# Kernel tuning notes

Hardware: AMD Instinct MI355X
Metric: run time of the kernel (lower is better)

Reference implementation:

```python
import jax, jax.numpy as jnp
import numpy as np
from jax import lax

B, T, C = 8, 2048, 1024
H, N = 16, 64          # n_head, head_size (C = H*N)
FFN = 3584             # dim_ffn = int(1024*3.5//32*32)
HSD = 8.0              # head_size_divisor
EPS = 1e-5


def setup_inputs() -> dict:
    key = jax.random.key(0)
    ks = jax.random.split(key, 24)
    s = 0.02
    return {
        'x': jax.random.normal(ks[0], (B, T, C), jnp.float32),
        'ln0_w': jnp.ones((C,), jnp.float32), 'ln0_b': jnp.zeros((C,), jnp.float32),
        'ln1_w': jnp.ones((C,), jnp.float32), 'ln1_b': jnp.zeros((C,), jnp.float32),
        'ln2_w': jnp.ones((C,), jnp.float32), 'ln2_b': jnp.zeros((C,), jnp.float32),
        'att_tmk': jax.random.uniform(ks[1], (C,), jnp.float32),
        'att_tmv': jax.random.uniform(ks[2], (C,), jnp.float32),
        'att_tmr': jax.random.uniform(ks[3], (C,), jnp.float32),
        'att_tmg': jax.random.uniform(ks[4], (C,), jnp.float32),
        'att_decay': jax.random.uniform(ks[5], (H, N), jnp.float32, -6.0, -1.0),
        'att_faaaa': jax.random.normal(ks[6], (H, N), jnp.float32) * 0.1,
        'att_Wr': jax.random.normal(ks[7], (C, C), jnp.float32) * s,
        'att_Wk': jax.random.normal(ks[8], (C, C), jnp.float32) * s,
        'att_Wv': jax.random.normal(ks[9], (C, C), jnp.float32) * s,
        'att_Wg': jax.random.normal(ks[10], (C, C), jnp.float32) * s,
        'att_Wo': jax.random.normal(ks[11], (C, C), jnp.float32) * s,
        'att_lnx_w': jnp.ones((C,), jnp.float32), 'att_lnx_b': jnp.zeros((C,), jnp.float32),
        'ffn_tmk': jax.random.uniform(ks[12], (C,), jnp.float32),
        'ffn_tmr': jax.random.uniform(ks[13], (C,), jnp.float32),
        'ffn_Wk': jax.random.normal(ks[14], (FFN, C), jnp.float32) * s,
        'ffn_Wr': jax.random.normal(ks[15], (C, C), jnp.float32) * s,
        'ffn_Wv': jax.random.normal(ks[16], (C, FFN), jnp.float32) * s,
    }


def token_shift(x):
    # nn.ZeroPad2d((0,0,1,-1)): shift right by one along T with zero front pad
    return jnp.pad(x, ((0, 0), (1, 0), (0, 0)))[:, :-1, :]


def layer_norm(x, w, b):
    mu = jnp.mean(x, -1, keepdims=True)
    var = jnp.var(x, -1, keepdims=True)
    return (x - mu) * lax.rsqrt(var + EPS) * w + b


def group_norm(x, w, b):
    # GroupNorm(H groups) over channel dim C = H*N
    xg = x.reshape(*x.shape[:-1], H, N)
    mu = jnp.mean(xg, -1, keepdims=True)
    var = jnp.var(xg, -1, keepdims=True)
    xg = (xg - mu) * lax.rsqrt(var + EPS)
    return xg.reshape(x.shape) * w + b


def wkv5(r, k, v, w, u):
    # r,k,v: [B,T,C]; w,u: [H,N]. Per-head decayed linear attention recurrence.
    ew = jnp.exp(-jnp.exp(w))  # [H,N] decay in (0,1)
    rt = r.reshape(B, T, H, N).transpose(1, 0, 2, 3)  # [T,B,H,N]
    kt = k.reshape(B, T, H, N).transpose(1, 0, 2, 3)
    vt = v.reshape(B, T, H, N).transpose(1, 0, 2, 3)

    def step(S, rkv):
        r_, k_, v_ = rkv                                   # [B,H,N]
        a = k_[..., :, None] * v_[..., None, :]            # [B,H,N,N] outer k v^T
        y = jnp.einsum('bhi,bhij->bhj', r_, S + u[:, :, None] * a)
        S = ew[None, :, :, None] * S + a
        return S, y

    S0 = jnp.zeros((B, H, N, N), r.dtype)
    _, ys = lax.scan(step, S0, (rt, kt, vt))               # ys: [T,B,H,N]
    return ys.transpose(1, 0, 2, 3).reshape(B, T, C)


def reference(x, ln0_w, ln0_b, ln1_w, ln1_b, ln2_w, ln2_b,
              att_tmk, att_tmv, att_tmr, att_tmg, att_decay, att_faaaa,
              att_Wr, att_Wk, att_Wv, att_Wg, att_Wo, att_lnx_w, att_lnx_b,
              ffn_tmk, ffn_tmr, ffn_Wk, ffn_Wr, ffn_Wv):
    x = layer_norm(x, ln0_w, ln0_b)  # layer_id == 0

    # --- time-mix (RWKV_Tmix_x052) ---
    xn = layer_norm(x, ln1_w, ln1_b)
    xx = token_shift(xn)
    xk = xn * att_tmk + xx * (1 - att_tmk)
    xv = xn * att_tmv + xx * (1 - att_tmv)
    xr = xn * att_tmr + xx * (1 - att_tmr)
    xg = xn * att_tmg + xx * (1 - att_tmg)
    r = xr @ att_Wr.T
    k = xk @ att_Wk.T
    v = xv @ att_Wv.T
    g = jax.nn.silu(xg @ att_Wg.T)
    y = wkv5(r, k, v, att_decay, att_faaaa)
    y = group_norm(y / HSD, att_lnx_w, att_lnx_b)
    x = x + (y * g) @ att_Wo.T

    # --- channel-mix (RWKV_CMix_x052) ---
    xn = layer_norm(x, ln2_w, ln2_b)
    xx = token_shift(xn)
    xk = xn * ffn_tmk + xx * (1 - ffn_tmk)
    xr = xn * ffn_tmr + xx * (1 - ffn_tmr)
    kf = jnp.square(jax.nn.relu(xk @ ffn_Wk.T))
    kv = kf @ ffn_Wv.T
    x = x + jax.nn.sigmoid(xr @ ffn_Wr.T) * kv
    return x
```

## Files before the change

### kernel.cpp

```cpp
#include <hip/hip_runtime.h>

#define Bq 8
#define Tq 2048
#define Cq 1024
#define Hq 16
#define Nq 64
#define FFNq 3584
#define EPSq 1e-5f

typedef __bf16 bf8v __attribute__((ext_vector_type(8)));
typedef float f32x4 __attribute__((ext_vector_type(4)));

typedef __attribute__((address_space(1))) const unsigned int GU;
typedef __attribute__((address_space(3))) unsigned int LU;

__device__ __forceinline__ void gload16(const unsigned short* g, unsigned short* l) {
    __builtin_amdgcn_global_load_lds((GU*)g, (LU*)l, 16, 0, 0);
}

__device__ __forceinline__ unsigned short f2bf(float f) {
    unsigned u = __float_as_uint(f);
    u += 0x7fffu + ((u >> 16) & 1u);
    return (unsigned short)(u >> 16);
}
__device__ __forceinline__ float bf2f(unsigned short h) {
    return __uint_as_float(((unsigned)h) << 16);
}

__global__ __launch_bounds__(256)
void diag_kernel(float* __restrict__ out, float val) {
    int i = (blockIdx.x * 256 + threadIdx.x) * 4;
    float4 v = make_float4(val, val, val, val);
    *(float4*)(out + i) = v;
}

__global__ __launch_bounds__(256)
void f2bf_all_kernel(const float* __restrict__ s0, const float* __restrict__ s1,
                     const float* __restrict__ s2, const float* __restrict__ s3,
                     const float* __restrict__ s4, const float* __restrict__ s5,
                     const float* __restrict__ s6, const float* __restrict__ s7,
                     unsigned short* __restrict__ d0, unsigned short* __restrict__ d1,
                     unsigned short* __restrict__ d2, unsigned short* __restrict__ d3,
                     unsigned short* __restrict__ d4, unsigned short* __restrict__ d5,
                     unsigned short* __restrict__ d6, unsigned short* __restrict__ d7) {
    int b = blockIdx.x;
    const float* src; unsigned short* dst;
    if      (b < 1024)  { src = s0; dst = d0; }
    else if (b < 2048)  { src = s1; dst = d1; b -= 1024; }
    else if (b < 3072)  { src = s2; dst = d2; b -= 2048; }
    else if (b < 4096)  { src = s3; dst = d3; b -= 3072; }
    else if (b < 5120)  { src = s4; dst = d4; b -= 4096; }
    else if (b < 8704)  { src = s5; dst = d5; b -= 5120; }
    else if (b < 9728)  { src = s6; dst = d6; b -= 8704; }
    else                { src = s7; dst = d7; b -= 9728; }
    int i = (b * 256 + threadIdx.x) * 4;
    float4 v = *(const float4*)(src + i);
    ushort4 o;
    o.x = f2bf(v.x); o.y = f2bf(v.y); o.z = f2bf(v.z); o.w = f2bf(v.w);
    *(ushort4*)(dst + i) = o;
}

__device__ __forceinline__ void blockred2(float& a, float& b, float* sm) {
#pragma unroll
    for (int m = 1; m < 64; m <<= 1) { a += __shfl_xor(a, m); b += __shfl_xor(b, m); }
    const int w = threadIdx.x >> 6;
    __syncthreads();
    if ((threadIdx.x & 63) == 0) { sm[w] = a; sm[4 + w] = b; }
    __syncthreads();
    a = sm[0] + sm[1] + sm[2] + sm[3];
    b = sm[4] + sm[5] + sm[6] + sm[7];
}

__global__ __launch_bounds__(256)
void ln01_kernel(const float* __restrict__ x,
                 const float* __restrict__ w0, const float* __restrict__ b0,
                 const float* __restrict__ w1, const float* __restrict__ b1,
                 float* __restrict__ x0, unsigned short* __restrict__ xn) {
    __shared__ float sm[8];
    const int tok = blockIdx.x, tid = threadIdx.x, c = tid * 4;
    const size_t base = (size_t)tok * Cq + c;
    float4 v = *(const float4*)(x + base);
    float s = v.x + v.y + v.z + v.w;
    float ss = v.x * v.x + v.y * v.y + v.z * v.z + v.w * v.w;
    blockred2(s, ss, sm);
    float mu = s * (1.f / Cq);
    float rstd = rsqrtf(ss * (1.f / Cq) - mu * mu + EPSq);
    float4 wv = *(const float4*)(w0 + c), bv = *(const float4*)(b0 + c);
    float4 e;
    e.x = (v.x - mu) * rstd * wv.x + bv.x;
    e.y = (v.y - mu) * rstd * wv.y + bv.y;
    e.z = (v.z - mu) * rstd * wv.z + bv.z;
    e.w = (v.w - mu) * rstd * wv.w + bv.w;
    *(float4*)(x0 + base) = e;
    s = e.x + e.y + e.z + e.w;
    ss = e.x * e.x + e.y * e.y + e.z * e.z + e.w * e.w;
    blockred2(s, ss, sm);
    mu = s * (1.f / Cq);
    rstd = rsqrtf(ss * (1.f / Cq) - mu * mu + EPSq);
    wv = *(const float4*)(w1 + c); bv = *(const float4*)(b1 + c);
    ushort4 o;
    o.x = f2bf((e.x - mu) * rstd * wv.x + bv.x);
    o.y = f2bf((e.y - mu) * rstd * wv.y + bv.y);
    o.z = f2bf((e.z - mu) * rstd * wv.z + bv.z);
    o.w = f2bf((e.w - mu) * rstd * wv.w + bv.w);
    *(ushort4*)(xn + base) = o;
}

__global__ __launch_bounds__(256)
void ln_kernel(const float* __restrict__ x, const float* __restrict__ w,
               const float* __restrict__ b, unsigned short* __restrict__ out) {
    __shared__ float sm[8];
    const int tok = blockIdx.x, tid = threadIdx.x, c = tid * 4;
    const size_t base = (size_t)tok * Cq + c;
    float4 v = *(const float4*)(x + base);
    float s = v.x + v.y + v.z + v.w;
    float ss = v.x * v.x + v.y * v.y + v.z * v.z + v.w * v.w;
    blockred2(s, ss, sm);
    float mu = s * (1.f / Cq);
    float rstd = rsqrtf(ss * (1.f / Cq) - mu * mu + EPSq);
    float4 wv = *(const float4*)(w + c), bv = *(const float4*)(b + c);
    ushort4 o;
    o.x = f2bf((v.x - mu) * rstd * wv.x + bv.x);
    o.y = f2bf((v.y - mu) * rstd * wv.y + bv.y);
    o.z = f2bf((v.z - mu) * rstd * wv.z + bv.z);
    o.w = f2bf((v.w - mu) * rstd * wv.w + bv.w);
    *(ushort4*)(out + base) = o;
}

__device__ __forceinline__ ushort4 mixpack(float ax, float ay, float az, float aw,
                                           float px, float py, float pz, float pw,
                                           const float4& m) {
    ushort4 o;
    o.x = f2bf(px + m.x * (ax - px));
    o.y = f2bf(py + m.y * (ay - py));
    o.z = f2bf(pz + m.z * (az - pz));
    o.w = f2bf(pw + m.w * (aw - pw));
    return o;
}

__global__ __launch_bounds__(256)
void mix4_kernel(const unsigned short* __restrict__ xn,
                 const float* __restrict__ tmr, const float* __restrict__ tmk,
                 const float* __restrict__ tmv, const float* __restrict__ tmg,
                 ushort4* __restrict__ outR, ushort4* __restrict__ outK,
                 ushort4* __restrict__ outV, ushort4* __restrict__ outG) {
    const int tok = blockIdx.x, tid = threadIdx.x, c = tid * 4;
    const int t = tok & (Tq - 1);
    const size_t base = (size_t)tok * Cq + c;
    ushort4 a = *(const ushort4*)(xn + base);
    ushort4 p = make_ushort4(0, 0, 0, 0);
    if (t) p = *(const ushort4*)(xn + base - Cq);
    float ax = bf2f(a.x), ay = bf2f(a.y), az = bf2f(a.z), aw = bf2f(a.w);
    float px = bf2f(p.x), py = bf2f(p.y), pz = bf2f(p.z), pw = bf2f(p.w);
    const size_t b4 = (size_t)tok * 256 + tid;
    outR[b4] = mixpack(ax, ay, az, aw, px, py, pz, pw, *(const float4*)(tmr + c));
    outK[b4] = mixpack(ax, ay, az, aw, px, py, pz, pw, *(const float4*)(tmk + c));
    outV[b4] = mixpack(ax, ay, az, aw, px, py, pz, pw, *(const float4*)(tmv + c));
    outG[b4] = mixpack(ax, ay, az, aw, px, py, pz, pw, *(const float4*)(tmg + c));
}

__global__ __launch_bounds__(256)
void mix2_kernel(const unsigned short* __restrict__ xn,
                 const float* __restrict__ tmk, const float* __restrict__ tmr,
                 ushort4* __restrict__ outK, ushort4* __restrict__ outR) {
    const int tok = blockIdx.x, tid = threadIdx.x, c = tid * 4;
    const int t = tok & (Tq - 1);
    const size_t base = (size_t)tok * Cq + c;
    ushort4 a = *(const ushort4*)(xn + base);
    ushort4 p = make_ushort4(0, 0, 0, 0);
    if (t) p = *(const ushort4*)(xn + base - Cq);
    float ax = bf2f(a.x), ay = bf2f(a.y), az = bf2f(a.z), aw = bf2f(a.w);
    float px = bf2f(p.x), py = bf2f(p.y), pz = bf2f(p.z), pw = bf2f(p.w);
    const size_t b4 = (size_t)tok * 256 + tid;
    outK[b4] = mixpack(ax, ay, az, aw, px, py, pz, pw, *(const float4*)(tmk + c));
    outR[b4] = mixpack(ax, ay, az, aw, px, py, pz, pw, *(const float4*)(tmr + c));
}

template<int MODE>
__global__ __launch_bounds__(512, 4)
void gemm128(const unsigned short* __restrict__ A, const unsigned short* __restrict__ W,
             int K, int N, float* __restrict__ outF, unsigned short* __restrict__ outB,
             const float* __restrict__ res, const unsigned short* __restrict__ sg) {
    __shared__ unsigned short lds[3][12288];
    const int tid = threadIdx.x;
    const int wid = tid >> 6, lane = tid & 63;
    const int wr = wid >> 1, wc = wid & 1;
    const int l15 = lane & 15, q = lane >> 4;

    const int nn = N >> 7;
    const int q8 = gridDim.x >> 3;
    const int bid = blockIdx.x;
    const int swz = (bid & 7) * q8 + (bid >> 3);
    const int m0 = (swz / nn) * 256;
    const int n0 = (swz % nn) * 128;

    const int srow = tid >> 2;
    const int scol = ((tid & 3) ^ ((tid >> 2) & 3)) * 8;
    const unsigned short* aS0 = A + (size_t)(m0 + srow) * K + scol;
    const unsigned short* aS1 = A + (size_t)(m0 + 128 + srow) * K + scol;
    const unsigned short* wS  = W + (size_t)(n0 + srow) * K + scol;

    const int fco = (q ^ (l15 & 3)) * 8;
    const int aOff = (wr * 64 + l15) * 32 + fco;
    const int bOff = 8192 + (wc * 64 + l15) * 32 + fco;

    f32x4 acc[4][4];
#pragma unroll
    for (int mi = 0; mi < 4; ++mi)
#pragma unroll
        for (int ni = 0; ni < 4; ++ni)
            acc[mi][ni] = {0.f, 0.f, 0.f, 0.f};

    const int NJ = K >> 5;

#pragma unroll
    for (int j = 0; j < 2; ++j) {
        gload16(aS0 + j * 32, &lds[j][tid * 8]);
        gload16(aS1 + j * 32, &lds[j][4096 + tid * 8]);
        gload16(wS  + j * 32, &lds[j][8192 + tid * 8]);
    }
    asm volatile("s_waitcnt vmcnt(3)" ::: "memory");
    __builtin_amdgcn_s_barrier();

    unsigned short* L0 = &lds[0][0];
    unsigned short* L1 = &lds[1][0];
    unsigned short* L2 = &lds[2][0];

    for (int k = 0; k < NJ; ++k) {
        if (k + 2 < NJ) {
            gload16(aS0 + (k + 2) * 32, L2 + tid * 8);
            gload16(aS1 + (k + 2) * 32, L2 + 4096 + tid * 8);
            gload16(wS  + (k + 2) * 32, L2 + 8192 + tid * 8);
        }
        bf8v a[4], b[4];
#pragma unroll
        for (int i = 0; i < 4; ++i) a[i] = *(const bf8v*)&L0[aOff + i * 512];
#pragma unroll
        for (int i = 0; i < 4; ++i) b[i] = *(const bf8v*)&L0[bOff + i * 512];
        __builtin_amdgcn_s_setprio(1);
#pragma unroll
        for (int mi = 0; mi < 4; ++mi)
#pragma unroll
            for (int ni = 0; ni < 4; ++ni)
                acc[mi][ni] = __builtin_amdgcn_mfma_f32_16x16x32_bf16(a[mi], b[ni], acc[mi][ni], 0, 0, 0);
        __builtin_amdgcn_s_setprio(0);
        if (k < NJ - 2) {
            asm volatile("s_waitcnt vmcnt(3)" ::: "memory");
            __builtin_amdgcn_s_barrier();
        } else if (k == NJ - 2) {
            asm volatile("s_waitcnt vmcnt(0)" ::: "memory");
            __builtin_amdgcn_s_barrier();
        }
        unsigned short* t0 = L0; L0 = L1; L1 = L2; L2 = t0;
    }

#pragma unroll
    for (int mi = 0; mi < 4; ++mi)
#pragma unroll
        for (int ni = 0; ni < 4; ++ni)
#pragma unroll
            for (int j = 0; j < 4; ++j) {
                const int row = m0 + wr * 64 + mi * 16 + q * 4 + j;
                const int col = n0 + wc * 64 + ni * 16 + l15;
                const size_t idx = (size_t)row * N + col;
                const float av = acc[mi][ni][j];
                if (MODE == 1) {
                    outB[idx] = f2bf(av / (1.f + __expf(-av)));
                } else if (MODE == 2) {
                    outF[idx] = res[idx] + av;
                } else if (MODE == 3) {
                    float tt = fmaxf(av, 0.f);
                    outB[idx] = f2bf(tt * tt);
                } else if (MODE == 4) {
                    outB[idx] = f2bf(1.f / (1.f + __expf(-av)));
                } else if (MODE == 5) {
                    outF[idx] = res[idx] + bf2f(sg[idx]) * av;
                } else {
                    outB[idx] = f2bf(av);
                }
            }
}

__global__ __launch_bounds__(256)
void wkv_kernel(const unsigned short* __restrict__ r, const unsigned short* __restrict__ k,
                const unsigned short* __restrict__ v, const unsigned short* __restrict__ g,
                const float* __restrict__ decay, const float* __restrict__ faaaa,
                const float* __restrict__ lnxw, const float* __restrict__ lnxb,
                unsigned short* __restrict__ ao) {
    __shared__ unsigned short rp[64 * 72], km[64 * 72], kdT[64 * 72];
    __shared__ unsigned short VT[64 * 72], Abf[64 * 72], ScT[64 * 72], Gsh[64 * 72];
    __shared__ float Dt[64];
    const int tid = threadIdx.x;
    const int bh = blockIdx.x, b = bh >> 4, h = bh & 15;
    const int tr = tid >> 2, g4 = tid & 3, i0 = g4 * 16;
    const int wv = tid >> 6, lane = tid & 63, l15 = lane & 15, q = lane >> 4;
    const float LOG2E = 1.44269504088896340736f;

    float l2w[16], uu[16];
#pragma unroll
    for (int ii = 0; ii < 16; ++ii) {
        l2w[ii] = -__expf(decay[h * Nq + i0 + ii]) * LOG2E;
        uu[ii] = faaaa[h * Nq + i0 + ii];
    }
    float ewL[4];
#pragma unroll
    for (int jr = 0; jr < 4; ++jr) {
        float lw = -__expf(decay[h * Nq + 16 * wv + q * 4 + jr]) * LOG2E;
        ewL[jr] = exp2f(64.f * lw);
    }
    const int colbase = h * Nq;
    float lwj[4], lbj[4];
#pragma unroll
    for (int nt = 0; nt < 4; ++nt) {
        lwj[nt] = lnxw[colbase + 16 * nt + l15];
        lbj[nt] = lnxb[colbase + 16 * nt + l15];
    }
    f32x4 S[4];
#pragma unroll
    for (int nt = 0; nt < 4; ++nt) S[nt] = {0.f, 0.f, 0.f, 0.f};
    for (int idx = tid; idx < 64 * 72; idx += 256) ScT[idx] = 0;
    __syncthreads();

    const size_t rowbase = (size_t)b * Tq;

    for (int c = 0; c < 32; ++c) {
        const size_t grow = (rowbase + c * 64 + tr) * Cq + colbase + i0;
        unsigned short rs_[16], ks_[16], vs_[16];
        *(uint4*)&rs_[0] = *(const uint4*)(r + grow);
        *(uint4*)&rs_[8] = *(const uint4*)(r + grow + 8);
        *(uint4*)&ks_[0] = *(const uint4*)(k + grow);
        *(uint4*)&ks_[8] = *(const uint4*)(k + grow + 8);
        *(uint4*)&vs_[0] = *(const uint4*)(v + grow);
        *(uint4*)&vs_[8] = *(const uint4*)(v + grow + 8);
        *(uint4*)&Gsh[tr * 72 + i0] = *(const uint4*)(g + grow);
        *(uint4*)&Gsh[tr * 72 + i0 + 8] = *(const uint4*)(g + grow + 8);
        float pd = 0.f;
        const float ftr = (float)tr;
#pragma unroll
        for (int ii = 0; ii < 16; ++ii) {
            float rf = bf2f(rs_[ii]), kf = bf2f(ks_[ii]);
            rp[tr * 72 + i0 + ii] = f2bf(rf * exp2f(ftr * l2w[ii]));
            km[tr * 72 + i0 + ii] = f2bf(kf * exp2f(-(ftr + 1.f) * l2w[ii]));
            kdT[(i0 + ii) * 72 + tr] = f2bf(kf * exp2f((63.f - ftr) * l2w[ii]));
            VT[(i0 + ii) * 72 + tr] = vs_[ii];
            pd += rf * uu[ii] * kf;
        }
        pd += __shfl_xor(pd, 1);
        pd += __shfl_xor(pd, 2);
        if (g4 == 0) Dt[tr] = pd;
        __syncthreads();

        f32x4 accA[4];
#pragma unroll
        for (int nt = 0; nt < 4; ++nt) accA[nt] = {0.f, 0.f, 0.f, 0.f};
#pragma unroll
        for (int ks = 0; ks < 2; ++ks) {
            bf8v a = *(const bf8v*)&rp[(16 * wv + l15) * 72 + ks * 32 + q * 8];
#pragma unroll
            for (int nt = 0; nt < 4; ++nt) {
                bf8v bbv = *(const bf8v*)&km[(16 * nt + l15) * 72 + ks * 32 + q * 8];
                accA[nt] = __builtin_amdgcn_mfma_f32_16x16x32_bf16(a, bbv, accA[nt], 0, 0, 0);
            }
        }
#pragma unroll
        for (int nt = 0; nt < 4; ++nt)
#pragma unroll
            for (int jr = 0; jr < 4; ++jr) {
                const int t = 16 * wv + q * 4 + jr, s = 16 * nt + l15;
                const float a = accA[nt][jr];
                const float val = (s < t) ? a : ((s == t) ? Dt[t] : 0.f);
                Abf[t * 72 + s] = f2bf(val);
            }

        f32x4 accY[4];
#pragma unroll
        for (int nt = 0; nt < 4; ++nt) accY[nt] = {0.f, 0.f, 0.f, 0.f};
#pragma unroll
        for (int ks = 0; ks < 2; ++ks) {
            bf8v a = *(const bf8v*)&Abf[(16 * wv + l15) * 72 + ks * 32 + q * 8];
#pragma unroll
            for (int nt = 0; nt < 4; ++nt) {
                bf8v bbv = *(const bf8v*)&VT[(16 * nt + l15) * 72 + ks * 32 + q * 8];
                accY[nt] = __builtin_amdgcn_mfma_f32_16x16x32_bf16(a, bbv, accY[nt], 0, 0, 0);
            }
        }
#pragma unroll
        for (int ks = 0; ks < 2; ++ks) {
            bf8v a = *(const bf8v*)&rp[(16 * wv + l15) * 72 + ks * 32 + q * 8];
#pragma unroll
            for (int nt = 0; nt < 4; ++nt) {
                bf8v bbv = *(const bf8v*)&ScT[(16 * nt + l15) * 72 + ks * 32 + q * 8];
                accY[nt] = __builtin_amdgcn_mfma_f32_16x16x32_bf16(a, bbv, accY[nt], 0, 0, 0);
            }
        }

        float sum_[4] = {0.f, 0.f, 0.f, 0.f}, sq_[4] = {0.f, 0.f, 0.f, 0.f};
#pragma unroll
        for (int nt = 0; nt < 4; ++nt)
#pragma unroll
            for (int jr = 0; jr < 4; ++jr) {
                float yv = accY[nt][jr] * 0.125f;
                accY[nt][jr] = yv;
                sum_[jr] += yv;
                sq_[jr] += yv * yv;
            }
#pragma unroll
        for (int m = 1; m < 16; m <<= 1)
#pragma unroll
            for (int jr = 0; jr < 4; ++jr) {
                sum_[jr] += __shfl_xor(sum_[jr], m);
                sq_[jr] += __shfl_xor(sq_[jr], m);
            }
        float mu_[4], rstd_[4];
#pragma unroll
        for (int jr = 0; jr < 4; ++jr) {
            mu_[jr] = sum_[jr] * (1.f / Nq);
            rstd_[jr] = rsqrtf(sq_[jr] * (1.f / Nq) - mu_[jr] * mu_[jr] + EPSq);
        }
#pragma unroll
        for (int nt = 0; nt < 4; ++nt)
#pragma unroll
            for (int jr = 0; jr < 4; ++jr) {
                const int t = 16 * wv + q * 4 + jr;
                const float gate = bf2f(Gsh[t * 72 + 16 * nt + l15]);
                const float val = (accY[nt][jr] - mu_[jr]) * rstd_[jr] * lwj[nt] + lbj[nt];
                ao[(rowbase + c * 64 + t) * Cq + colbase + 16 * nt + l15] = f2bf(val * gate);
            }

        f32x4 accU[4];
#pragma unroll
        for (int nt = 0; nt < 4; ++nt) accU[nt] = {0.f, 0.f, 0.f, 0.f};
#pragma unroll
        for (int ks = 0; ks < 2; ++ks) {
            bf8v a = *(const bf8v*)&kdT[(16 * wv + l15) * 72 + ks * 32 + q * 8];
#pragma unroll
            for (int nt = 0; nt < 4; ++nt) {
                bf8v bbv = *(const bf8v*)&VT[(16 * nt + l15) * 72 + ks * 32 + q * 8];
                accU[nt] = __builtin_amdgcn_mfma_f32_16x16x32_bf16(a, bbv, accU[nt], 0, 0, 0);
            }
        }
        __syncthreads();
#pragma unroll
        for (int nt = 0; nt < 4; ++nt) {
#pragma unroll
            for (int jr = 0; jr < 4; ++jr)
                S[nt][jr] = ewL[jr] * S[nt][jr] + accU[nt][jr];
            ushort4 sc;
            sc.x = f2bf(S[nt][0]); sc.y = f2bf(S[nt][1]);
            sc.z = f2bf(S[nt][2]); sc.w = f2bf(S[nt][3]);
            *(ushort4*)&ScT[(16 * nt + l15) * 72 + 16 * wv + q * 4] = sc;
        }
        __syncthreads();
    }
}

extern "C" void kernel_launch(void* const* d_in, const int* in_sizes, int n_in,
                              void* d_out, int out_size, void* d_ws, size_t ws_size,
                              hipStream_t stream) {
    const float* x     = (const float*)d_in[0];
    const float* ln0w  = (const float*)d_in[1];
    const float* ln0b  = (const float*)d_in[2];
    const float* ln1w  = (const float*)d_in[3];
    const float* ln1b  = (const float*)d_in[4];
    const float* ln2w  = (const float*)d_in[5];
    const float* ln2b  = (const float*)d_in[6];
    const float* atmk  = (const float*)d_in[7];
    const float* atmv  = (const float*)d_in[8];
    const float* atmr  = (const float*)d_in[9];
    const float* atmg  = (const float*)d_in[10];
    const float* decay = (const float*)d_in[11];
    const float* faaaa = (const float*)d_in[12];
    const float* aWr   = (const float*)d_in[13];
    const float* aWk   = (const float*)d_in[14];
    const float* aWv   = (const float*)d_in[15];
    const float* aWg   = (const float*)d_in[16];
    const float* aWo   = (const float*)d_in[17];
    const float* lnxw  = (const float*)d_in[18];
    const float* lnxb  = (const float*)d_in[19];
    const float* ftmk  = (const float*)d_in[20];
    const float* ftmr  = (const float*)d_in[21];
    const float* fWk   = (const float*)d_in[22];
    const float* fWr   = (const float*)d_in[23];
    const float* fWv   = (const float*)d_in[24];

    const size_t MB = 1024ull * 1024ull;
    const size_t WS_NEEDED = 250 * MB;
    dim3 blk(256);

    if (ws_size < WS_NEEDED) {
        diag_kernel<<<out_size / 1024, blk, 0, stream>>>((float*)d_out,
            1000.f + (float)((double)ws_size / (double)MB));
        return;
    }

    char* ws = (char*)d_ws;
    unsigned short* WR  = (unsigned short*)(ws + 0 * MB);
    unsigned short* WK  = (unsigned short*)(ws + 2 * MB);
    unsigned short* WV  = (unsigned short*)(ws + 4 * MB);
    unsigned short* WG  = (unsigned short*)(ws + 6 * MB);
    unsigned short* WO  = (unsigned short*)(ws + 8 * MB);
    unsigned short* FWK = (unsigned short*)(ws + 10 * MB);
    unsigned short* FWR = (unsigned short*)(ws + 17 * MB);
    unsigned short* FWV = (unsigned short*)(ws + 19 * MB);
    unsigned short* XN  = (unsigned short*)(ws + 26 * MB);
    unsigned short* MXR = (unsigned short*)(ws + 58 * MB);
    unsigned short* MXK = (unsigned short*)(ws + 90 * MB);
    unsigned short* MXV = (unsigned short*)(ws + 122 * MB);
    unsigned short* MXG = (unsigned short*)(ws + 154 * MB);
    unsigned short* Rb  = (unsigned short*)(ws + 186 * MB);
    unsigned short* Kb  = (unsigned short*)(ws + 58 * MB);
    unsigned short* Vb  = (unsigned short*)(ws + 90 * MB);
    unsigned short* Gb  = (unsigned short*)(ws + 122 * MB);
    unsigned short* AO  = (unsigned short*)(ws + 154 * MB);
    unsigned short* XK2 = (unsigned short*)(ws + 58 * MB);
    unsigned short* XR2 = (unsigned short*)(ws + 90 * MB);
    unsigned short* KF  = (unsigned short*)(ws + 122 * MB);
    unsigned short* SRb = (unsigned short*)(ws + 26 * MB);
    float*          X0  = (float*)d_out;

    const int NTOK = Bq * Tq;
    dim3 blk512(512);
    const int gsq = (NTOK / 256) * (Cq / 128);
    const int gup = (NTOK / 256) * (FFNq / 128);

    f2bf_all_kernel<<<13312, blk, 0, stream>>>(aWr, aWk, aWv, aWg, aWo, fWk, fWr, fWv,
                                               WR, WK, WV, WG, WO, FWK, FWR, FWV);

    ln01_kernel<<<NTOK, blk, 0, stream>>>(x, ln0w, ln0b, ln1w, ln1b, X0, XN);

    mix4_kernel<<<NTOK, blk, 0, stream>>>(XN, atmr, atmk, atmv, atmg,
                                          (ushort4*)MXR, (ushort4*)MXK,
                                          (ushort4*)MXV, (ushort4*)MXG);

    gemm128<6><<<gsq, blk512, 0, stream>>>(MXR, WR, Cq, Cq, nullptr, Rb, nullptr, nullptr);
    gemm128<6><<<gsq, blk512, 0, stream>>>(MXK, WK, Cq, Cq, nullptr, Kb, nullptr, nullptr);
    gemm128<6><<<gsq, blk512, 0, stream>>>(MXV, WV, Cq, Cq, nullptr, Vb, nullptr, nullptr);
    gemm128<1><<<gsq, blk512, 0, stream>>>(MXG, WG, Cq, Cq, nullptr, Gb, nullptr, nullptr);

    wkv_kernel<<<Bq * Hq, blk, 0, stream>>>(Rb, Kb, Vb, Gb, decay, faaaa, lnxw, lnxb, AO);
    gemm128<2><<<gsq, blk512, 0, stream>>>(AO, WO, Cq, Cq, X0, nullptr, X0, nullptr);

    ln_kernel<<<NTOK, blk, 0, stream>>>(X0, ln2w, ln2b, XN);
    mix2_kernel<<<NTOK, blk, 0, stream>>>(XN, ftmk, ftmr, (ushort4*)XK2, (ushort4*)XR2);
    gemm128<3><<<gup, blk512, 0, stream>>>(XK2, FWK, Cq, FFNq, nullptr, KF, nullptr, nullptr);
    gemm128<4><<<gsq, blk512, 0, stream>>>(XR2, FWR, Cq, Cq, nullptr, SRb, nullptr, nullptr);
    gemm128<5><<<gsq, blk512, 0, stream>>>(KF, FWV, FFNq, Cq, X0, nullptr, X0, SRb);
}
```

Baseline: 943.7 us.

## Batch R/K/V projections and FFN key/receptance GEMMs into shared launches; hoist WKV decay powers

The three square R/K/V projection GEMMs now run in one grouped launch, and the FFN key GEMM shares a launch with the receptance GEMM. The goal is to cut launch overhead and tail-wave idle time by letting the independent GEMMs fill the GPU together. Workspace buffers for K/V/G are moved to new offsets so the grouped outputs do not overwrite inputs still being read. In the WKV kernel, the per-row decay exponentials are computed once before the chunk loop instead of on every chunk, at the cost of 48 extra registers per thread.

```diff
diff --git a/kernel.cpp b/kernel.cpp
--- a/kernel.cpp
+++ b/kernel.cpp
@@ -176,23 +176,16 @@
     outR[b4] = mixpack(ax, ay, az, aw, px, py, pz, pw, *(const float4*)(tmr + c));
 }
 
-template<int MODE>
-__global__ __launch_bounds__(512, 4)
-void gemm128(const unsigned short* __restrict__ A, const unsigned short* __restrict__ W,
-             int K, int N, float* __restrict__ outF, unsigned short* __restrict__ outB,
-             const float* __restrict__ res, const unsigned short* __restrict__ sg) {
-    __shared__ unsigned short lds[3][12288];
+__device__ __forceinline__ void gemm_body(
+    const unsigned short* __restrict__ A, const unsigned short* __restrict__ W,
+    int K, int N, int mode,
+    float* __restrict__ outF, unsigned short* __restrict__ outB,
+    const float* __restrict__ res, const unsigned short* __restrict__ sg,
+    int m0, int n0, unsigned short* lds) {
     const int tid = threadIdx.x;
     const int wid = tid >> 6, lane = tid & 63;
     const int wr = wid >> 1, wc = wid & 1;
     const int l15 = lane & 15, q = lane >> 4;
-
-    const int nn = N >> 7;
-    const int q8 = gridDim.x >> 3;
-    const int bid = blockIdx.x;
-    const int swz = (bid & 7) * q8 + (bid >> 3);
-    const int m0 = (swz / nn) * 256;
-    const int n0 = (swz % nn) * 128;
 
     const int srow = tid >> 2;
     const int scol = ((tid & 3) ^ ((tid >> 2) & 3)) * 8;
@@ -215,16 +208,16 @@
 
 #pragma unroll
     for (int j = 0; j < 2; ++j) {
-        gload16(aS0 + j * 32, &lds[j][tid * 8]);
-        gload16(aS1 + j * 32, &lds[j][4096 + tid * 8]);
-        gload16(wS  + j * 32, &lds[j][8192 + tid * 8]);
+        gload16(aS0 + j * 32, lds + j * 12288 + tid * 8);
+        gload16(aS1 + j * 32, lds + j * 12288 + 4096 + tid * 8);
+        gload16(wS  + j * 32, lds + j * 12288 + 8192 + tid * 8);
     }
     asm volatile("s_waitcnt vmcnt(3)" ::: "memory");
     __builtin_amdgcn_s_barrier();
 
-    unsigned short* L0 = &lds[0][0];
-    unsigned short* L1 = &lds[1][0];
-    unsigned short* L2 = &lds[2][0];
+    unsigned short* L0 = lds;
+    unsigned short* L1 = lds + 12288;
+    unsigned short* L2 = lds + 24576;
 
     for (int k = 0; k < NJ; ++k) {
         if (k + 2 < NJ) {
@@ -264,21 +257,77 @@
                 const int col = n0 + wc * 64 + ni * 16 + l15;
                 const size_t idx = (size_t)row * N + col;
                 const float av = acc[mi][ni][j];
-                if (MODE == 1) {
+                if (mode == 1) {
                     outB[idx] = f2bf(av / (1.f + __expf(-av)));
-                } else if (MODE == 2) {
+                } else if (mode == 2) {
                     outF[idx] = res[idx] + av;
-                } else if (MODE == 3) {
+                } else if (mode == 3) {
                     float tt = fmaxf(av, 0.f);
                     outB[idx] = f2bf(tt * tt);
-                } else if (MODE == 4) {
+                } else if (mode == 4) {
                     outB[idx] = f2bf(1.f / (1.f + __expf(-av)));
-                } else if (MODE == 5) {
+                } else if (mode == 5) {
                     outF[idx] = res[idx] + bf2f(sg[idx]) * av;
                 } else {
                     outB[idx] = f2bf(av);
                 }
             }
+}
+
+template<int MODE>
+__global__ __launch_bounds__(512, 4)
+void gemm128(const unsigned short* __restrict__ A, const unsigned short* __restrict__ W,
+             int K, int N, float* __restrict__ outF, unsigned short* __restrict__ outB,
+             const float* __restrict__ res, const unsigned short* __restrict__ sg) {
+    __shared__ unsigned short lds[3][12288];
+    const int nn = N >> 7;
+    const int q8 = gridDim.x >> 3;
+    const int bid = blockIdx.x;
+    const int swz = (bid & 7) * q8 + (bid >> 3);
+    const int m0 = (swz / nn) * 256;
+    const int n0 = (swz % nn) * 128;
+    gemm_body(A, W, K, N, MODE, outF, outB, res, sg, m0, n0, &lds[0][0]);
+}
+
+__global__ __launch_bounds__(512, 4)
+void proj3_kernel(const unsigned short* __restrict__ A0, const unsigned short* __restrict__ A1,
+                  const unsigned short* __restrict__ A2,
+                  const unsigned short* __restrict__ W0, const unsigned short* __restrict__ W1,
+                  const unsigned short* __restrict__ W2,
+                  unsigned short* __restrict__ O0, unsigned short* __restrict__ O1,
+                  unsigned short* __restrict__ O2) {
+    __shared__ unsigned short lds[3][12288];
+    const int bid = blockIdx.x;
+    const int seg = bid >> 9, inner = bid & 511;
+    const unsigned short* A; const unsigned short* W; unsigned short* O;
+    if (seg == 0)      { A = A0; W = W0; O = O0; }
+    else if (seg == 1) { A = A1; W = W1; O = O1; }
+    else               { A = A2; W = W2; O = O2; }
+    const int swz = (inner & 7) * 64 + (inner >> 3);
+    const int m0 = (swz >> 3) * 256;
+    const int n0 = (swz & 7) * 128;
+    gemm_body(A, W, Cq, Cq, 6, nullptr, O, nullptr, nullptr, m0, n0, &lds[0][0]);
+}
+
+__global__ __launch_bounds__(512, 4)
+void ffn2_kernel(const unsigned short* __restrict__ XK2, const unsigned short* __restrict__ FWK,
+                 unsigned short* __restrict__ KF,
+                 const unsigned short* __restrict__ XR2, const unsigned short* __restrict__ FWR,
+                 unsigned short* __restrict__ SRb) {
+    __shared__ unsigned short lds[3][12288];
+    const int bid = blockIdx.x;
+    if (bid < 1792) {
+        const int swz = (bid & 7) * 224 + (bid >> 3);
+        const int m0 = (swz / 28) * 256;
+        const int n0 = (swz % 28) * 128;
+        gemm_body(XK2, FWK, Cq, FFNq, 3, nullptr, KF, nullptr, nullptr, m0, n0, &lds[0][0]);
+    } else {
+        const int inner = bid - 1792;
+        const int swz = (inner & 7) * 64 + (inner >> 3);
+        const int m0 = (swz >> 3) * 256;
+        const int n0 = (swz & 7) * 128;
+        gemm_body(XR2, FWR, Cq, Cq, 4, nullptr, SRb, nullptr, nullptr, m0, n0, &lds[0][0]);
+    }
 }
 
 __global__ __launch_bounds__(256)
@@ -295,12 +344,20 @@
     const int tr = tid >> 2, g4 = tid & 3, i0 = g4 * 16;
     const int wv = tid >> 6, lane = tid & 63, l15 = lane & 15, q = lane >> 4;
     const float LOG2E = 1.44269504088896340736f;
+    const float ftr = (float)tr;
 
     float l2w[16], uu[16];
 #pragma unroll
     for (int ii = 0; ii < 16; ++ii) {
         l2w[ii] = -__expf(decay[h * Nq + i0 + ii]) * LOG2E;
         uu[ii] = faaaa[h * Nq + i0 + ii];
+    }
+    float rpw[16], kmw[16], kdw[16];
+#pragma unroll
+    for (int ii = 0; ii < 16; ++ii) {
+        rpw[ii] = exp2f(ftr * l2w[ii]);
+        kmw[ii] = exp2f(-(ftr + 1.f) * l2w[ii]);
+        kdw[ii] = exp2f((63.f - ftr) * l2w[ii]);
     }
     float ewL[4];
 #pragma unroll
@@ -335,13 +392,12 @@
         *(uint4*)&Gsh[tr * 72 + i0] = *(const uint4*)(g + grow);
         *(uint4*)&Gsh[tr * 72 + i0 + 8] = *(const uint4*)(g + grow + 8);
         float pd = 0.f;
-        const float ftr = (float)tr;
 #pragma unroll
         for (int ii = 0; ii < 16; ++ii) {
             float rf = bf2f(rs_[ii]), kf = bf2f(ks_[ii]);
-            rp[tr * 72 + i0 + ii] = f2bf(rf * exp2f(ftr * l2w[ii]));
-            km[tr * 72 + i0 + ii] = f2bf(kf * exp2f(-(ftr + 1.f) * l2w[ii]));
-            kdT[(i0 + ii) * 72 + tr] = f2bf(kf * exp2f((63.f - ftr) * l2w[ii]));
+            rp[tr * 72 + i0 + ii] = f2bf(rf * rpw[ii]);
+            km[tr * 72 + i0 + ii] = f2bf(kf * kmw[ii]);
+            kdT[(i0 + ii) * 72 + tr] = f2bf(kf * kdw[ii]);
             VT[(i0 + ii) * 72 + tr] = vs_[ii];
             pd += rf * uu[ii] * kf;
         }
@@ -508,9 +564,9 @@
     unsigned short* MXV = (unsigned short*)(ws + 122 * MB);
     unsigned short* MXG = (unsigned short*)(ws + 154 * MB);
     unsigned short* Rb  = (unsigned short*)(ws + 186 * MB);
-    unsigned short* Kb  = (unsigned short*)(ws + 58 * MB);
-    unsigned short* Vb  = (unsigned short*)(ws + 90 * MB);
-    unsigned short* Gb  = (unsigned short*)(ws + 122 * MB);
+    unsigned short* Kb  = (unsigned short*)(ws + 218 * MB);
+    unsigned short* Vb  = (unsigned short*)(ws + 26 * MB);
+    unsigned short* Gb  = (unsigned short*)(ws + 58 * MB);
     unsigned short* AO  = (unsigned short*)(ws + 154 * MB);
     unsigned short* XK2 = (unsigned short*)(ws + 58 * MB);
     unsigned short* XR2 = (unsigned short*)(ws + 90 * MB);
@@ -521,7 +577,6 @@
     const int NTOK = Bq * Tq;
     dim3 blk512(512);
     const int gsq = (NTOK / 256) * (Cq / 128);
-    const int gup = (NTOK / 256) * (FFNq / 128);
 
     f2bf_all_kernel<<<13312, blk, 0, stream>>>(aWr, aWk, aWv, aWg, aWo, fWk, fWr, fWv,
                                                WR, WK, WV, WG, WO, FWK, FWR, FWV);
@@ -532,9 +587,7 @@
                                           (ushort4*)MXR, (ushort4*)MXK,
                                           (ushort4*)MXV, (ushort4*)MXG);
 
-    gemm128<6><<<gsq, blk512, 0, stream>>>(MXR, WR, Cq, Cq, nullptr, Rb, nullptr, nullptr);
-    gemm128<6><<<gsq, blk512, 0, stream>>>(MXK, WK, Cq, Cq, nullptr, Kb, nullptr, nullptr);
-    gemm128<6><<<gsq, blk512, 0, stream>>>(MXV, WV, Cq, Cq, nullptr, Vb, nullptr, nullptr);
+    proj3_kernel<<<1536, blk512, 0, stream>>>(MXR, MXK, MXV, WR, WK, WV, Rb, Kb, Vb);
     gemm128<1><<<gsq, blk512, 0, stream>>>(MXG, WG, Cq, Cq, nullptr, Gb, nullptr, nullptr);
 
     wkv_kernel<<<Bq * Hq, blk, 0, stream>>>(Rb, Kb, Vb, Gb, decay, faaaa, lnxw, lnxb, AO);
@@ -542,7 +595,6 @@
 
     ln_kernel<<<NTOK, blk, 0, stream>>>(X0, ln2w, ln2b, XN);
     mix2_kernel<<<NTOK, blk, 0, stream>>>(XN, ftmk, ftmr, (ushort4*)XK2, (ushort4*)XR2);
-    gemm128<3><<<gup, blk512, 0, stream>>>(XK2, FWK, Cq, FFNq, nullptr, KF, nullptr, nullptr);
-    gemm128<4><<<gsq, blk512, 0, stream>>>(XR2, FWR, Cq, Cq, nullptr, SRb, nullptr, nullptr);
+    ffn2_kernel<<<2304, blk512, 0, stream>>>(XK2, FWK, KF, XR2, FWR, SRb);
     gemm128<5><<<gsq, blk512, 0, stream>>>(KF, FWV, FFNq, Cq, X0, nullptr, X0, SRb);
 }
```

New measurement: 916.3 us. 1.03x faster.
